# Kernel tuning notes

Hardware: AMD Instinct MI355X
Metric: run time of the kernel (lower is better)

The kernel has to match this reference:

```python
import jax, jax.numpy as jnp
import numpy as np

B, S, DIN, DOUT = 4, 2048, 4096, 4096

def setup_inputs() -> dict:
    key = jax.random.key(0)
    k1, k2, k3, k4 = jax.random.split(key, 4)
    x = jax.random.normal(k1, (B, S, DIN), dtype=jnp.float32)
    # int8-valued weights stored in int32 (harness dtype constraint); values in [-127, 127]
    weight_int8 = jax.random.randint(k2, (DOUT, DIN), -127, 128, dtype=jnp.int32)
    # per-output-channel scales, small positive values typical of int8 quantization
    scale = jax.random.uniform(k3, (DOUT,), dtype=jnp.float32, minval=1e-4, maxval=2e-2)
    bias = jax.random.normal(k4, (DOUT,), dtype=jnp.float32)
    return {"x": x, "weight_int8": weight_int8, "scale": scale, "bias": bias}

def reference(x, weight_int8, scale, bias):
    # Dequantize: w[o, i] = int8[o, i] * scale[o], cast to activation dtype
    w = (weight_int8.astype(jnp.float32) * scale[:, None]).astype(x.dtype)  # [DOUT, DIN]
    # F.linear: y = x @ w.T + bias
    return jnp.einsum('bsi,oi->bso', x, w) + bias
```

## Files before the change

kernel.cpp:

```cpp
#include <hip/hip_runtime.h>
#include <hip/hip_bf16.h>

#define BM 256
#define BN 256
#define BK 64
#define NSLOT 4
#define LDS_BYTES (2 * NSLOT * BM * BK)

typedef float  f32x4  __attribute__((ext_vector_type(4)));
typedef int    i32x4  __attribute__((ext_vector_type(4)));
typedef __bf16 bf16x8 __attribute__((ext_vector_type(8)));
typedef __bf16 bf16x4 __attribute__((ext_vector_type(4)));

__device__ __forceinline__ void gload_lds16(const void* g, void* l) {
    __builtin_amdgcn_global_load_lds(
        (const __attribute__((address_space(1))) void*)g,
        (__attribute__((address_space(3))) void*)l, 16, 0, 0);
}

__global__ __launch_bounds__(256)
void rowquant_x(const float* __restrict__ x, signed char* __restrict__ xq,
                float* __restrict__ xs, int K) {
    const int row = blockIdx.x;
    const float* xr = x + (size_t)row * K;
    const int tid = threadIdx.x;
    const int n4 = K / 4;

    float mx = 0.f;
    for (int i = tid; i < n4; i += 256) {
        f32x4 v = ((const f32x4*)xr)[i];
        mx = fmaxf(mx, fmaxf(fmaxf(fabsf(v[0]), fabsf(v[1])),
                             fmaxf(fabsf(v[2]), fabsf(v[3]))));
    }
#pragma unroll
    for (int off = 32; off; off >>= 1)
        mx = fmaxf(mx, __shfl_xor(mx, off));
    __shared__ float smx[4];
    if ((tid & 63) == 0) smx[tid >> 6] = mx;
    __syncthreads();
    mx = fmaxf(fmaxf(smx[0], smx[1]), fmaxf(smx[2], smx[3]));

    const float inv = mx > 0.f ? 127.f / mx : 0.f;
    if (tid == 0) xs[row] = mx / 127.f;

    unsigned* out = (unsigned*)(xq + (size_t)row * K);
    for (int i = tid; i < n4; i += 256) {
        f32x4 v = ((const f32x4*)xr)[i];
        int q0 = __float2int_rn(v[0] * inv);
        int q1 = __float2int_rn(v[1] * inv);
        int q2 = __float2int_rn(v[2] * inv);
        int q3 = __float2int_rn(v[3] * inv);
        out[i] = (unsigned)(q0 & 255) | ((unsigned)(q1 & 255) << 8) |
                 ((unsigned)(q2 & 255) << 16) | ((unsigned)(q3 & 255) << 24);
    }
}

__global__ __launch_bounds__(256)
void cvt_w_i8(const int* __restrict__ w, unsigned* __restrict__ wq, int n4) {
    int i = blockIdx.x * 256 + threadIdx.x;
    const int stride = gridDim.x * 256;
    for (; i < n4; i += stride) {
        i32x4 v = ((const i32x4*)w)[i];
        wq[i] = (unsigned)(v[0] & 255) | ((unsigned)(v[1] & 255) << 8) |
                ((unsigned)(v[2] & 255) << 16) | ((unsigned)(v[3] & 255) << 24);
    }
}


__global__ __launch_bounds__(512, 2)
void qlin_gemm_i8(const signed char* __restrict__ A,
                  const signed char* __restrict__ B,
                  const float* __restrict__ xs,
                  const float* __restrict__ scale,
                  const float* __restrict__ bias,
                  float* __restrict__ C, int M, int N, int K) {
    extern __shared__ signed char lds[];
    signed char* lA = lds;
    signed char* lB = lds + NSLOT * (BM * BK);

    const int NTN = N / BN;
    const int nwg = gridDim.x;
    int bid = blockIdx.x;
    bid = (bid & 7) * (nwg >> 3) + (bid >> 3);
    const int tm = bid / NTN;
    const int tn = bid % NTN;

    const int tid  = threadIdx.x;
    const int lane = tid & 63;
    const int wid  = tid >> 6;
    const int wr   = wid >> 2;
    const int wc   = wid & 3;

    const int srow0 = wid * 32 + (lane >> 2);
    const int srow1 = srow0 + 16;
    const int gq0 = (lane & 3) ^ ((srow0 >> 1) & 3);
    const int gq1 = (lane & 3) ^ ((srow1 >> 1) & 3);
    const signed char* Ap0 = A + (size_t)(tm * BM + srow0) * K + gq0 * 16;
    const signed char* Ap1 = A + (size_t)(tm * BM + srow1) * K + gq1 * 16;
    const signed char* Bp0 = B + (size_t)(tn * BN + srow0) * K + gq0 * 16;
    const signed char* Bp1 = B + (size_t)(tn * BN + srow1) * K + gq1 * 16;

    const int NT = K / BK;

    auto STAGE_A = [&](int t) {
        signed char* d = lA + (t & (NSLOT - 1)) * (BM * BK) + wid * 2048;
        gload_lds16(Ap0 + t * BK, d);
        gload_lds16(Ap1 + t * BK, d + 1024);
    };
    auto STAGE_B = [&](int t) {
        signed char* d = lB + (t & (NSLOT - 1)) * (BM * BK) + wid * 2048;
        gload_lds16(Bp0 + t * BK, d);
        gload_lds16(Bp1 + t * BK, d + 1024);
    };

    const int fr = lane & 15;
    const int kq = lane >> 4;

    auto AOFF = [&](int mi) {
        const int R = wr * 128 + mi * 16 + fr;
        return R * 64 + ((kq ^ ((R >> 1) & 3)) << 4);
    };
    auto BOFF = [&](int ni) {
        const int R = wc * 64 + ni * 16 + fr;
        return R * 64 + ((kq ^ ((R >> 1) & 3)) << 4);
    };

    i32x4 acc[8][4];
#pragma unroll
    for (int mi = 0; mi < 8; ++mi)
#pragma unroll
        for (int ni = 0; ni < 4; ++ni) {
            acc[mi][ni][0] = 0; acc[mi][ni][1] = 0;
            acc[mi][ni][2] = 0; acc[mi][ni][3] = 0;
        }

    for (int u = 0; u < 3 && u < NT; ++u) { STAGE_A(u); STAGE_B(u); }

    for (int t = 0; t < NT; ++t) {
        const signed char* lAs = lA + (t & (NSLOT - 1)) * (BM * BK);
        const signed char* lBs = lB + (t & (NSLOT - 1)) * (BM * BK);
        const int rem = NT - 1 - t;

        if (rem >= 2)      asm volatile("s_waitcnt vmcnt(8)" ::: "memory");
        else if (rem == 1) asm volatile("s_waitcnt vmcnt(4)" ::: "memory");
        else               asm volatile("s_waitcnt vmcnt(0)" ::: "memory");
        __builtin_amdgcn_s_barrier();

        i32x4 af[8], bf[4];
#pragma unroll
        for (int mi = 0; mi < 8; ++mi)
            af[mi] = *(const i32x4*)(lAs + AOFF(mi));
#pragma unroll
        for (int ni = 0; ni < 4; ++ni)
            bf[ni] = *(const i32x4*)(lBs + BOFF(ni));

        if (t + 3 < NT) { STAGE_A(t + 3); STAGE_B(t + 3); }

        __builtin_amdgcn_s_setprio(1);
#pragma unroll
        for (int mi = 0; mi < 8; ++mi)
#pragma unroll
            for (int ni = 0; ni < 4; ++ni)
                acc[mi][ni] = __builtin_amdgcn_mfma_i32_16x16x64_i8(
                    af[mi], bf[ni], acc[mi][ni], 0, 0, 0);
        __builtin_amdgcn_s_setprio(0);
    }

    const int rb = tm * BM + wr * 128 + (lane >> 4) * 4;
    const int cb = tn * BN + wc * 64 + fr;
#pragma unroll
    for (int mi = 0; mi < 8; ++mi) {
        const int m0 = rb + mi * 16;
        float sm[4];
#pragma unroll
        for (int r = 0; r < 4; ++r) sm[r] = xs[m0 + r];
#pragma unroll
        for (int ni = 0; ni < 4; ++ni) {
            const int n = cb + ni * 16;
            const float sc = scale[n];
            const float bs = bias[n];
#pragma unroll
            for (int r = 0; r < 4; ++r)
                C[(size_t)(m0 + r) * N + n] =
                    fmaf((float)acc[mi][ni][r], sm[r] * sc, bs);
        }
    }
}

#define FBM 128
#define FBK 32

__device__ __forceinline__ int swz_elem(int row, int e) {
    return row * FBK + (e ^ (((row >> 1) & 3) << 3));
}

__global__ __launch_bounds__(256, 2)
void qlin_gemm_reg(const float* __restrict__ A, const int* __restrict__ W,
                   const float* __restrict__ scale, const float* __restrict__ bias,
                   float* __restrict__ C, int M, int N, int K) {
    __shared__ __bf16 lA[2][FBM * FBK];
    __shared__ __bf16 lB[2][FBM * FBK];
    const int NTN = N / FBM;
    const int nwg = gridDim.x;
    int bid = blockIdx.x;
    if ((nwg & 7) == 0) bid = (bid & 7) * (nwg >> 3) + (bid >> 3);
    const int tm = bid / NTN, tn = bid % NTN;
    const int tid = threadIdx.x, lane = tid & 63, wid = tid >> 6;
    const int wr = wid >> 1, wc = wid & 1;
    const int srow0 = tid >> 3, skq = tid & 7;
    const float* aptr = A + (size_t)(tm * FBM + srow0) * K + skq * 4;
    const int*   wptr = W + (size_t)(tn * FBM + srow0) * K + skq * 4;
    const size_t rstride = (size_t)32 * K;
    f32x4 sa[4]; i32x4 sw[4];
    auto LOAD = [&](int t) {
#pragma unroll
        for (int j = 0; j < 4; ++j) {
            sa[j] = *(const f32x4*)(aptr + (size_t)t * FBK + j * rstride);
            sw[j] = *(const i32x4*)(wptr + (size_t)t * FBK + j * rstride);
        }
    };
    auto STORE = [&](int buf) {
#pragma unroll
        for (int j = 0; j < 4; ++j) {
            const int idx = swz_elem(srow0 + j * 32, skq * 4);
            bf16x4 va = { (__bf16)sa[j][0], (__bf16)sa[j][1],
                          (__bf16)sa[j][2], (__bf16)sa[j][3] };
            bf16x4 vw = { (__bf16)(float)sw[j][0], (__bf16)(float)sw[j][1],
                          (__bf16)(float)sw[j][2], (__bf16)(float)sw[j][3] };
            *(bf16x4*)&lA[buf][idx] = va;
            *(bf16x4*)&lB[buf][idx] = vw;
        }
    };
    const f32x4 fzero = {0.f, 0.f, 0.f, 0.f};
    f32x4 acc[4][4];
#pragma unroll
    for (int i = 0; i < 4; ++i)
#pragma unroll
        for (int j = 0; j < 4; ++j) acc[i][j] = fzero;
    const int fr = lane & 15, fks = (lane >> 4) * 8;
    LOAD(0); STORE(0); __syncthreads();
    const int NT = K / FBK;
    for (int t = 0; t < NT; ++t) {
        const int buf = t & 1;
        if (t + 1 < NT) LOAD(t + 1);
        bf16x8 af[4], bfg[4];
#pragma unroll
        for (int mi = 0; mi < 4; ++mi)
            af[mi] = *(const bf16x8*)&lA[buf][swz_elem(wr * 64 + mi * 16 + fr, fks)];
#pragma unroll
        for (int ni = 0; ni < 4; ++ni)
            bfg[ni] = *(const bf16x8*)&lB[buf][swz_elem(wc * 64 + ni * 16 + fr, fks)];
#pragma unroll
        for (int mi = 0; mi < 4; ++mi)
#pragma unroll
            for (int ni = 0; ni < 4; ++ni)
                acc[mi][ni] = __builtin_amdgcn_mfma_f32_16x16x32_bf16(
                    af[mi], bfg[ni], acc[mi][ni], 0, 0, 0);
        if (t + 1 < NT) STORE(buf ^ 1);
        __syncthreads();
    }
    const int row0 = tm * FBM + wr * 64 + (lane >> 4) * 4;
    const int col0 = tn * FBM + wc * 64 + fr;
#pragma unroll
    for (int ni = 0; ni < 4; ++ni) {
        const int n = col0 + ni * 16;
        const float sc = scale[n], bs = bias[n];
#pragma unroll
        for (int mi = 0; mi < 4; ++mi) {
            const int m = row0 + mi * 16;
#pragma unroll
            for (int r = 0; r < 4; ++r)
                C[(size_t)(m + r) * N + n] = fmaf(acc[mi][ni][r], sc, bs);
        }
    }
}

extern "C" void kernel_launch(void* const* d_in, const int* in_sizes, int n_in,
                              void* d_out, int out_size, void* d_ws, size_t ws_size,
                              hipStream_t stream) {
    const float* x     = (const float*)d_in[0];
    const int*   w8    = (const int*)d_in[1];
    const float* scale = (const float*)d_in[2];
    const float* bias  = (const float*)d_in[3];
    float*       out   = (float*)d_out;

    const int DOUT = in_sizes[2];
    const int DIN  = in_sizes[1] / DOUT;
    const int M    = in_sizes[0] / DIN;

    const size_t need = (size_t)M * DIN + (size_t)DOUT * DIN + (size_t)M * 4;
    const int nwg = (M / BM) * (DOUT / BN);
    const bool ok = (ws_size >= need) && (M % BM == 0) && (DOUT % BN == 0) &&
                    (DIN % BK == 0) && (nwg % 8 == 0) && (DIN / BK >= 4);
    if (ok) {
        signed char* xq = (signed char*)d_ws;
        signed char* wq = xq + (size_t)M * DIN;
        float*       xs = (float*)(wq + (size_t)DOUT * DIN);
        rowquant_x<<<M, 256, 0, stream>>>(x, xq, xs, DIN);
        cvt_w_i8<<<2048, 256, 0, stream>>>(w8, (unsigned*)wq, DOUT * DIN / 4);
        hipFuncSetAttribute(reinterpret_cast<const void*>(qlin_gemm_i8),
                            hipFuncAttributeMaxDynamicSharedMemorySize, LDS_BYTES);
        qlin_gemm_i8<<<nwg, 512, LDS_BYTES, stream>>>(xq, wq, xs, scale, bias, out,
                                                      M, DOUT, DIN);
    } else {
        dim3 grid((M / FBM) * (DOUT / FBM));
        qlin_gemm_reg<<<grid, 256, 0, stream>>>(x, w8, scale, bias, out, M, DOUT, DIN);
    }
}
```

Before: 191.6 us.

## Shrink int8 GEMM tiles to 128x128 with double-buffered LDS and 256 threads

Reduces the int8 GEMM tile from 256x256 to 128x128, uses 4 waves per block instead of 8, and replaces the 4-slot, 3-ahead prefetch pipeline with a simple 2-slot double buffer that waits on all loads each iteration. The aim is more workgroups per CU and a better-filled grid. In exchange it lowers data reuse per tile, roughly doubling global/LDS traffic per MFMA, and weakens latency hiding because of the full vmcnt(0) wait before each barrier.

```diff
diff --git a/kernel.cpp b/kernel.cpp
--- a/kernel.cpp
+++ b/kernel.cpp
@@ -1,11 +1,11 @@
 #include <hip/hip_runtime.h>
 #include <hip/hip_bf16.h>
 
-#define BM 256
-#define BN 256
+#define BM 128
+#define BN 128
 #define BK 64
-#define NSLOT 4
-#define LDS_BYTES (2 * NSLOT * BM * BK)
+#define NSLOT 2
+#define LDS_BYTES (NSLOT * (BM + BN) * BK)
 
 typedef float  f32x4  __attribute__((ext_vector_type(4)));
 typedef int    i32x4  __attribute__((ext_vector_type(4)));
@@ -67,7 +67,7 @@
 }
 
 
-__global__ __launch_bounds__(512, 2)
+__global__ __launch_bounds__(256, 3)
 void qlin_gemm_i8(const signed char* __restrict__ A,
                   const signed char* __restrict__ B,
                   const float* __restrict__ xs,
@@ -88,36 +88,31 @@
     const int tid  = threadIdx.x;
     const int lane = tid & 63;
     const int wid  = tid >> 6;
-    const int wr   = wid >> 2;
-    const int wc   = wid & 3;
-
-    const int srow0 = wid * 32 + (lane >> 2);
-    const int srow1 = srow0 + 16;
-    const int gq0 = (lane & 3) ^ ((srow0 >> 1) & 3);
-    const int gq1 = (lane & 3) ^ ((srow1 >> 1) & 3);
-    const signed char* Ap0 = A + (size_t)(tm * BM + srow0) * K + gq0 * 16;
-    const signed char* Ap1 = A + (size_t)(tm * BM + srow1) * K + gq1 * 16;
-    const signed char* Bp0 = B + (size_t)(tn * BN + srow0) * K + gq0 * 16;
-    const signed char* Bp1 = B + (size_t)(tn * BN + srow1) * K + gq1 * 16;
+    const int wr   = wid >> 1;
+    const int wc   = wid & 1;
+
+    const int srow = wid * 16 + (lane >> 2);
+    const int gq   = (lane & 3) ^ ((srow >> 1) & 3);
+    const signed char* Ap = A + (size_t)(tm * BM + srow) * K + gq * 16;
+    const signed char* Bp = B + (size_t)(tn * BN + srow) * K + gq * 16;
+    const size_t jstride = (size_t)64 * K;
 
     const int NT = K / BK;
 
-    auto STAGE_A = [&](int t) {
-        signed char* d = lA + (t & (NSLOT - 1)) * (BM * BK) + wid * 2048;
-        gload_lds16(Ap0 + t * BK, d);
-        gload_lds16(Ap1 + t * BK, d + 1024);
-    };
-    auto STAGE_B = [&](int t) {
-        signed char* d = lB + (t & (NSLOT - 1)) * (BM * BK) + wid * 2048;
-        gload_lds16(Bp0 + t * BK, d);
-        gload_lds16(Bp1 + t * BK, d + 1024);
+    auto STAGE = [&](int t) {
+        signed char* dA = lA + (t & 1) * (BM * BK) + wid * 1024;
+        signed char* dB = lB + (t & 1) * (BM * BK) + wid * 1024;
+        gload_lds16(Ap + t * BK, dA);
+        gload_lds16(Ap + t * BK + jstride, dA + 4096);
+        gload_lds16(Bp + t * BK, dB);
+        gload_lds16(Bp + t * BK + jstride, dB + 4096);
     };
 
     const int fr = lane & 15;
     const int kq = lane >> 4;
 
     auto AOFF = [&](int mi) {
-        const int R = wr * 128 + mi * 16 + fr;
+        const int R = wr * 64 + mi * 16 + fr;
         return R * 64 + ((kq ^ ((R >> 1) & 3)) << 4);
     };
     auto BOFF = [&](int ni) {
@@ -125,40 +120,37 @@
         return R * 64 + ((kq ^ ((R >> 1) & 3)) << 4);
     };
 
-    i32x4 acc[8][4];
-#pragma unroll
-    for (int mi = 0; mi < 8; ++mi)
+    i32x4 acc[4][4];
+#pragma unroll
+    for (int mi = 0; mi < 4; ++mi)
 #pragma unroll
         for (int ni = 0; ni < 4; ++ni) {
             acc[mi][ni][0] = 0; acc[mi][ni][1] = 0;
             acc[mi][ni][2] = 0; acc[mi][ni][3] = 0;
         }
 
-    for (int u = 0; u < 3 && u < NT; ++u) { STAGE_A(u); STAGE_B(u); }
+    STAGE(0);
 
     for (int t = 0; t < NT; ++t) {
-        const signed char* lAs = lA + (t & (NSLOT - 1)) * (BM * BK);
-        const signed char* lBs = lB + (t & (NSLOT - 1)) * (BM * BK);
-        const int rem = NT - 1 - t;
-
-        if (rem >= 2)      asm volatile("s_waitcnt vmcnt(8)" ::: "memory");
-        else if (rem == 1) asm volatile("s_waitcnt vmcnt(4)" ::: "memory");
-        else               asm volatile("s_waitcnt vmcnt(0)" ::: "memory");
+        const signed char* lAs = lA + (t & 1) * (BM * BK);
+        const signed char* lBs = lB + (t & 1) * (BM * BK);
+
+        asm volatile("s_waitcnt vmcnt(0) lgkmcnt(0)" ::: "memory");
         __builtin_amdgcn_s_barrier();
 
-        i32x4 af[8], bf[4];
-#pragma unroll
-        for (int mi = 0; mi < 8; ++mi)
+        if (t + 1 < NT) STAGE(t + 1);
+
+        i32x4 af[4], bf[4];
+#pragma unroll
+        for (int mi = 0; mi < 4; ++mi)
             af[mi] = *(const i32x4*)(lAs + AOFF(mi));
 #pragma unroll
         for (int ni = 0; ni < 4; ++ni)
             bf[ni] = *(const i32x4*)(lBs + BOFF(ni));
 
-        if (t + 3 < NT) { STAGE_A(t + 3); STAGE_B(t + 3); }
-
         __builtin_amdgcn_s_setprio(1);
 #pragma unroll
-        for (int mi = 0; mi < 8; ++mi)
+        for (int mi = 0; mi < 4; ++mi)
 #pragma unroll
             for (int ni = 0; ni < 4; ++ni)
                 acc[mi][ni] = __builtin_amdgcn_mfma_i32_16x16x64_i8(
@@ -166,10 +158,10 @@
         __builtin_amdgcn_s_setprio(0);
     }
 
-    const int rb = tm * BM + wr * 128 + (lane >> 4) * 4;
+    const int rb = tm * BM + wr * 64 + (lane >> 4) * 4;
     const int cb = tn * BN + wc * 64 + fr;
 #pragma unroll
-    for (int mi = 0; mi < 8; ++mi) {
+    for (int mi = 0; mi < 4; ++mi) {
         const int m0 = rb + mi * 16;
         float sm[4];
 #pragma unroll
@@ -291,7 +283,7 @@
     const size_t need = (size_t)M * DIN + (size_t)DOUT * DIN + (size_t)M * 4;
     const int nwg = (M / BM) * (DOUT / BN);
     const bool ok = (ws_size >= need) && (M % BM == 0) && (DOUT % BN == 0) &&
-                    (DIN % BK == 0) && (nwg % 8 == 0) && (DIN / BK >= 4);
+                    (DIN % BK == 0) && (nwg % 8 == 0) && (DIN / BK >= 2);
     if (ok) {
         signed char* xq = (signed char*)d_ws;
         signed char* wq = xq + (size_t)M * DIN;
@@ -300,7 +292,7 @@
         cvt_w_i8<<<2048, 256, 0, stream>>>(w8, (unsigned*)wq, DOUT * DIN / 4);
         hipFuncSetAttribute(reinterpret_cast<const void*>(qlin_gemm_i8),
                             hipFuncAttributeMaxDynamicSharedMemorySize, LDS_BYTES);
-        qlin_gemm_i8<<<nwg, 512, LDS_BYTES, stream>>>(xq, wq, xs, scale, bias, out,
+        qlin_gemm_i8<<<nwg, 256, LDS_BYTES, stream>>>(xq, wq, xs, scale, bias, out,
                                                       M, DOUT, DIN);
     } else {
         dim3 grid((M / FBM) * (DOUT / FBM));
```

Result: slower. 241.7 us (+26.2%).

## Interleave LDS fragment loads with MFMA phases in int8 GEMM main loop

Applied to the files above, without the earlier changes.

Splits each K-step into four phases. Each phase loads two A fragments from LDS while the previous pair's MFMAs run, and the STAGE_A and STAGE_B global-to-LDS copies are spread across phases. The goal is to overlap LDS read latency with matrix-core work and to lower register pressure by holding only two A fragments at a time. In exchange it adds extra workgroup barriers and full lgkmcnt(0) waits per phase, which could serialize waves.

```diff
diff --git a/kernel.cpp b/kernel.cpp
--- a/kernel.cpp
+++ b/kernel.cpp
@@ -136,6 +136,24 @@
 
     for (int u = 0; u < 3 && u < NT; ++u) { STAGE_A(u); STAGE_B(u); }
 
+#define PH_MFMA(M0, A0v, A1v)                                               \
+    __builtin_amdgcn_s_setprio(1);                                          \
+    acc[M0][0] = __builtin_amdgcn_mfma_i32_16x16x64_i8(A0v, bf0, acc[M0][0], 0, 0, 0); \
+    acc[M0][1] = __builtin_amdgcn_mfma_i32_16x16x64_i8(A0v, bf1, acc[M0][1], 0, 0, 0); \
+    acc[M0][2] = __builtin_amdgcn_mfma_i32_16x16x64_i8(A0v, bf2, acc[M0][2], 0, 0, 0); \
+    acc[M0][3] = __builtin_amdgcn_mfma_i32_16x16x64_i8(A0v, bf3, acc[M0][3], 0, 0, 0); \
+    acc[M0+1][0] = __builtin_amdgcn_mfma_i32_16x16x64_i8(A1v, bf0, acc[M0+1][0], 0, 0, 0); \
+    acc[M0+1][1] = __builtin_amdgcn_mfma_i32_16x16x64_i8(A1v, bf1, acc[M0+1][1], 0, 0, 0); \
+    acc[M0+1][2] = __builtin_amdgcn_mfma_i32_16x16x64_i8(A1v, bf2, acc[M0+1][2], 0, 0, 0); \
+    acc[M0+1][3] = __builtin_amdgcn_mfma_i32_16x16x64_i8(A1v, bf3, acc[M0+1][3], 0, 0, 0); \
+    __builtin_amdgcn_s_setprio(0);
+
+#define LGKM0_FENCE                                                         \
+    asm volatile("s_waitcnt lgkmcnt(0)" ::: "memory");                      \
+    __builtin_amdgcn_sched_barrier(0);
+
+    i32x4 bf0, bf1, bf2, bf3, aE0, aE1, aO0, aO1;
+
     for (int t = 0; t < NT; ++t) {
         const signed char* lAs = lA + (t & (NSLOT - 1)) * (BM * BK);
         const signed char* lBs = lB + (t & (NSLOT - 1)) * (BM * BK);
@@ -146,25 +164,37 @@
         else               asm volatile("s_waitcnt vmcnt(0)" ::: "memory");
         __builtin_amdgcn_s_barrier();
 
-        i32x4 af[8], bf[4];
-#pragma unroll
-        for (int mi = 0; mi < 8; ++mi)
-            af[mi] = *(const i32x4*)(lAs + AOFF(mi));
-#pragma unroll
-        for (int ni = 0; ni < 4; ++ni)
-            bf[ni] = *(const i32x4*)(lBs + BOFF(ni));
-
-        if (t + 3 < NT) { STAGE_A(t + 3); STAGE_B(t + 3); }
-
-        __builtin_amdgcn_s_setprio(1);
-#pragma unroll
-        for (int mi = 0; mi < 8; ++mi)
-#pragma unroll
-            for (int ni = 0; ni < 4; ++ni)
-                acc[mi][ni] = __builtin_amdgcn_mfma_i32_16x16x64_i8(
-                    af[mi], bf[ni], acc[mi][ni], 0, 0, 0);
-        __builtin_amdgcn_s_setprio(0);
-    }
+        bf0 = *(const i32x4*)(lBs + BOFF(0));
+        bf1 = *(const i32x4*)(lBs + BOFF(1));
+        bf2 = *(const i32x4*)(lBs + BOFF(2));
+        bf3 = *(const i32x4*)(lBs + BOFF(3));
+        aE0 = *(const i32x4*)(lAs + AOFF(0));
+        aE1 = *(const i32x4*)(lAs + AOFF(1));
+        if (t + 3 < NT) STAGE_A(t + 3);
+        LGKM0_FENCE
+        PH_MFMA(0, aE0, aE1)
+        aO0 = *(const i32x4*)(lAs + AOFF(2));
+        aO1 = *(const i32x4*)(lAs + AOFF(3));
+        if (t + 3 < NT) STAGE_B(t + 3);
+        __builtin_amdgcn_s_barrier();
+
+        LGKM0_FENCE
+        PH_MFMA(2, aO0, aO1)
+        aE0 = *(const i32x4*)(lAs + AOFF(4));
+        aE1 = *(const i32x4*)(lAs + AOFF(5));
+        __builtin_amdgcn_s_barrier();
+
+        LGKM0_FENCE
+        PH_MFMA(4, aE0, aE1)
+        aO0 = *(const i32x4*)(lAs + AOFF(6));
+        aO1 = *(const i32x4*)(lAs + AOFF(7));
+        __builtin_amdgcn_s_barrier();
+
+        LGKM0_FENCE
+        PH_MFMA(6, aO0, aO1)
+    }
+#undef PH_MFMA
+#undef LGKM0_FENCE
 
     const int rb = tm * BM + wr * 128 + (lane >> 4) * 4;
     const int cb = tn * BN + wc * 64 + fr;
```

After: 195.4 us. No clear change (+2.0%).
